# Kernel tuning notes

Measured on AMD Instinct MI355X. Metric: run time of the kernel, lower is better.

The kernel has to match this reference:

```python
import jax, jax.numpy as jnp
import numpy as np

N_NODES = 32768
N_EDGES = 524288
IN_F = 256
OUT_F = 128
NB = 4


def setup_inputs() -> dict:
    key = jax.random.key(0)
    ks = jax.random.split(key, 12)
    s_in = 1.0 / np.sqrt(IN_F)
    s_out = 1.0 / np.sqrt(OUT_F)
    s_cat = 1.0 / np.sqrt(OUT_F * NB)
    return {
        "x": jax.random.normal(ks[0], (N_NODES, IN_F), dtype=jnp.float32),
        "edge_index": jax.random.randint(ks[1], (2, N_EDGES), 0, N_NODES, dtype=jnp.int64),
        "Wb": jax.random.uniform(ks[2], (NB, IN_F, OUT_F), jnp.float32, -s_in, s_in),
        "bb": jax.random.uniform(ks[3], (NB, OUT_F), jnp.float32, -s_in, s_in),
        "W1": jax.random.uniform(ks[4], (NB, OUT_F, OUT_F), jnp.float32, -s_out, s_out),
        "b1": jax.random.uniform(ks[5], (NB, OUT_F), jnp.float32, -s_out, s_out),
        "W2": jax.random.uniform(ks[6], (NB, OUT_F, OUT_F), jnp.float32, -s_out, s_out),
        "b2": jax.random.uniform(ks[7], (NB, OUT_F), jnp.float32, -s_out, s_out),
        "branch_gates": jnp.ones((NB,), dtype=jnp.float32),
        "temperature": jnp.asarray(1.0, dtype=jnp.float32),
        "Wo": jax.random.uniform(ks[8], (OUT_F * NB, OUT_F), jnp.float32, -s_cat, s_cat),
        "bo": jax.random.uniform(ks[9], (OUT_F,), jnp.float32, -s_cat, s_cat),
    }


def _scatter_mean_step(h, row, col, inv_deg):
    # gather per-edge source features, mean-reduce onto destination nodes
    sums = jax.ops.segment_sum(h[row], col, num_segments=N_NODES)
    return sums * inv_deg


def reference(x, edge_index, Wb, bb, W1, b1, W2, b2, branch_gates, temperature, Wo, bo):
    row, col = edge_index[0], edge_index[1]
    deg = jax.ops.segment_sum(jnp.ones((N_EDGES,), x.dtype), col, num_segments=N_NODES)
    inv_deg = (1.0 / jnp.maximum(deg, 1.0))[:, None]  # empty segments -> 0 (scatter_mean semantics)

    gates = jax.nn.softmax(branch_gates / temperature)

    branch_outputs = []
    for i in range(NB):
        h = x @ Wb[i] + bb[i]                   # [N, OUT_F]
        for _ in range(i):                       # scale = scales[i % 4] = i
            h = _scatter_mean_step(h, row, col, inv_deg)
        h = jax.nn.relu(h @ W1[i] + b1[i]) @ W2[i] + b2[i]
        branch_outputs.append(h * gates[i])

    concat = jnp.concatenate(branch_outputs, axis=1)  # [N, NB*OUT_F]
    return concat @ Wo + bo
```

## Files before the change

kernel.cpp:

```cpp
#include <hip/hip_runtime.h>
#include <math.h>

#define N_NODES 32768
#define N_EDGES 524288
#define IN_F    256
#define OUT_F   128
#define NB      4
#define STRIDE  96

#define NE_BLK   256
#define CONV_BLK 1024
#define GX_BLK   2048
#define GEMM_BLK (N_NODES / 128)
#define M_BLK    (N_NODES / 256)

typedef __attribute__((ext_vector_type(8))) short bf16x8;
typedef __attribute__((ext_vector_type(4))) float f32x4;
typedef __attribute__((ext_vector_type(4))) ushort u16x4;

__device__ __forceinline__ ushort f2b(float f) {
    uint u = __float_as_uint(f);
    return (ushort)((u + 0x7fffu + ((u >> 16) & 1u)) >> 16);
}
__device__ __forceinline__ float b2f_lo(uint v) { return __uint_as_float(v << 16); }
__device__ __forceinline__ float b2f_hi(uint v) { return __uint_as_float(v & 0xffff0000u); }

__device__ __forceinline__ float softmax_gate(const float* bg, const float* temp, int i) {
    float T = temp[0];
    float mx = fmaxf(fmaxf(bg[0], bg[1]), fmaxf(bg[2], bg[3]));
    float e0 = expf((bg[0] - mx) / T), e1 = expf((bg[1] - mx) / T);
    float e2 = expf((bg[2] - mx) / T), e3 = expf((bg[3] - mx) / T);
    float s = e0 + e1 + e2 + e3;
    float ei = (i == 0) ? e0 : (i == 1) ? e1 : (i == 2) ? e2 : e3;
    return ei / s;
}

__device__ __forceinline__ int detect_i32(const int* __restrict__ ei, int* sflag) {
    if (threadIdx.x < 64) {
        unsigned long long b = __ballot(ei[2 * threadIdx.x + 1] != 0);
        if (threadIdx.x == 0) *sflag = (b != 0ull) ? 1 : 0;
    }
    __syncthreads();
    return *sflag;
}

__global__ __launch_bounds__(256) void fill_all_kernel(
    const int* __restrict__ ei, int* __restrict__ cursor, ushort* __restrict__ srcs,
    const float* __restrict__ x, ushort* __restrict__ xb,
    const float* __restrict__ Wb, const float* __restrict__ W1,
    const float* __restrict__ W2, const float* __restrict__ Wo,
    const float* __restrict__ bb, const float* __restrict__ b2,
    const float* __restrict__ bo, const float* __restrict__ bg,
    const float* __restrict__ temp,
    ushort* __restrict__ WcT, ushort* __restrict__ WzT,
    float* __restrict__ u, float* __restrict__ cvec) {
    __shared__ float smem[16 * 128];
    __shared__ int sflag;
    int b = blockIdx.x;
    int tid = threadIdx.x;
    if (b < NE_BLK) {
        int i32 = detect_i32(ei, &sflag);
#pragma unroll
        for (int it = 0; it < 8; it++) {
            int e = b * 2048 + it * 256 + tid;
            int r, c;
            if (i32 == 0) {
                r = __builtin_nontemporal_load(ei + 2 * e);
                c = __builtin_nontemporal_load(ei + 2 * (N_EDGES + e));
            } else {
                r = __builtin_nontemporal_load(ei + e);
                c = __builtin_nontemporal_load(ei + N_EDGES + e);
            }
            int slot = atomicAdd(&cursor[c], 1);
            if (slot < STRIDE) srcs[(size_t)c * STRIDE + slot] = (ushort)r;
        }
        return;
    }
    b -= NE_BLK;
    if (b < CONV_BLK) {
#pragma unroll
        for (int it = 0; it < 8; it++) {
            int idx = b * 2048 + it * 256 + tid;
            f32x4 v = __builtin_nontemporal_load((const f32x4*)x + idx);
            u16x4 o;
            o.x = f2b(v.x); o.y = f2b(v.y); o.z = f2b(v.z); o.w = f2b(v.w);
            *((u16x4*)xb + idx) = o;
        }
        return;
    }
    b -= CONV_BLK;
    int f = tid & 127, rh = tid >> 7;
    if (b < 64) {
        int i = b >> 4, k0 = (b & 15) * 16;
#pragma unroll
        for (int rr = 0; rr < 8; rr++)
            smem[(rh * 8 + rr) * 128 + f] = Wb[((size_t)i * IN_F + k0 + rh * 8 + rr) * OUT_F + f];
        __syncthreads();
        float acc[8] = {};
        const float* W1i = W1 + (size_t)i * OUT_F * OUT_F;
        for (int j = 0; j < OUT_F; j++) {
            float w1 = W1i[j * OUT_F + f];
#pragma unroll
            for (int rr = 0; rr < 8; rr++) acc[rr] += smem[(rh * 8 + rr) * 128 + j] * w1;
        }
        ushort tmp[8];
#pragma unroll
        for (int rr = 0; rr < 8; rr++) tmp[rr] = f2b(acc[rr]);
        *(uint4*)(WcT + ((size_t)i * OUT_F + f) * IN_F + k0 + rh * 8) = *(uint4*)tmp;
    } else if (b < 96) {
        int id = b - 64;
        int i = id >> 3, j0 = (id & 7) * 16;
#pragma unroll
        for (int rr = 0; rr < 8; rr++)
            smem[(rh * 8 + rr) * 128 + f] = W2[((size_t)i * OUT_F + j0 + rh * 8 + rr) * OUT_F + f];
        __syncthreads();
        float acc[8] = {};
        for (int l = 0; l < OUT_F; l++) {
            float wo = Wo[((size_t)i * OUT_F + l) * OUT_F + f];
#pragma unroll
            for (int rr = 0; rr < 8; rr++) acc[rr] += smem[(rh * 8 + rr) * 128 + l] * wo;
        }
        float g = softmax_gate(bg, temp, i);
        ushort tmp[8];
#pragma unroll
        for (int rr = 0; rr < 8; rr++) tmp[rr] = f2b(g * acc[rr]);
        *(uint4*)(WzT + (size_t)f * (NB * OUT_F) + i * OUT_F + j0 + rh * 8) = *(uint4*)tmp;
    } else {
        int id = b - 96;
        int jc = rh;
        if (id < NB) {
            int i = id;
            float partial = 0.f;
            for (int j = jc * 64; j < jc * 64 + 64; j++)
                partial += bb[i * OUT_F + j] * W1[((size_t)i * OUT_F + j) * OUT_F + f];
            smem[jc * 128 + f] = partial;
            __syncthreads();
            if (jc == 0) u[i * OUT_F + f] = smem[f] + smem[128 + f];
        } else {
            int i = id - NB;
            float partial = 0.f;
            for (int j = jc * 64; j < jc * 64 + 64; j++)
                partial += b2[i * OUT_F + j] * Wo[((size_t)i * OUT_F + j) * OUT_F + f];
            smem[jc * 128 + f] = partial;
            __syncthreads();
            if (jc == 0) {
                float tot = (smem[f] + smem[128 + f]) * softmax_gate(bg, temp, i);
                if (i == 0) tot += bo[f];
                atomicAdd(&cvec[f], tot);
            }
        }
    }
}

#define ACC4(A, V)                                                              \
    A[0] += b2f_lo(V.x); A[1] += b2f_hi(V.x);                                   \
    A[2] += b2f_lo(V.y); A[3] += b2f_hi(V.y)

#define GATHER_SLICE(INBUF, ROWSTRIDE)                                          \
    float a0[4] = {0.f,0.f,0.f,0.f};                                            \
    float a1[4] = {0.f,0.f,0.f,0.f};                                            \
    int p = s;                                                                  \
    for (; p + 12 <= e; p += 12) {                                              \
        int base = p + 6 * half;                                                \
        uint s01 = *(const uint*)(srcs + base);                                 \
        uint s23 = *(const uint*)(srcs + base + 2);                             \
        uint s45 = *(const uint*)(srcs + base + 4);                             \
        uint2 v0 = *(const uint2*)(INBUF + (size_t)(s01 & 0xffffu) * ROWSTRIDE + colOff); \
        uint2 v1 = *(const uint2*)(INBUF + (size_t)(s01 >> 16)    * ROWSTRIDE + colOff); \
        uint2 v2 = *(const uint2*)(INBUF + (size_t)(s23 & 0xffffu) * ROWSTRIDE + colOff); \
        uint2 v3 = *(const uint2*)(INBUF + (size_t)(s23 >> 16)    * ROWSTRIDE + colOff); \
        uint2 v4 = *(const uint2*)(INBUF + (size_t)(s45 & 0xffffu) * ROWSTRIDE + colOff); \
        uint2 v5 = *(const uint2*)(INBUF + (size_t)(s45 >> 16)    * ROWSTRIDE + colOff); \
        ACC4(a0, v0); ACC4(a1, v1); ACC4(a0, v2);                               \
        ACC4(a1, v3); ACC4(a0, v4); ACC4(a1, v5);                               \
    }                                                                           \
    for (; p + 4 <= e; p += 4) {                                                \
        uint ss = *(const uint*)(srcs + p + 2 * half);                          \
        uint2 v0 = *(const uint2*)(INBUF + (size_t)(ss & 0xffffu) * ROWSTRIDE + colOff); \
        uint2 v1 = *(const uint2*)(INBUF + (size_t)(ss >> 16)    * ROWSTRIDE + colOff); \
        ACC4(a0, v0); ACC4(a1, v1);                                             \
    }                                                                           \
    for (; p + half < e; p += 2) {                                              \
        int src = srcs[p + half];                                               \
        uint2 v0 = *(const uint2*)(INBUF + (size_t)src * ROWSTRIDE + colOff);   \
        ACC4(a0, v0);                                                           \
    }                                                                           \
    _Pragma("unroll") for (int k = 0; k < 4; k++) a0[k] += a1[k];               \
    _Pragma("unroll") for (int k = 0; k < 4; k++) a0[k] += __shfl_down(a0[k], 32);

#define PACK2(A, W)                                                             \
    { o.x = (uint)f2b(A[0] * W) | ((uint)f2b(A[1] * W) << 16);                  \
      o.y = (uint)f2b(A[2] * W) | ((uint)f2b(A[3] * W) << 16); }

__global__ __launch_bounds__(256, 8) void prop_x_kernel(
    const ushort* __restrict__ xb, ushort* __restrict__ X1b,
    const int* __restrict__ deg, float* __restrict__ m2,
    const ushort* __restrict__ srcs) {
    int blk = blockIdx.x;
    int tid = threadIdx.x;
    if (blk < M_BLK) {
        int n = blk * 256 + tid;
        int d = deg[n];
        int s = n * STRIDE, e = s + ((d < STRIDE) ? d : STRIDE);
        float sum = 0.f;
        for (int p = s; p < e; ++p) sum += (deg[srcs[p]] > 0) ? 1.0f : 0.0f;
        m2[n] = sum / (float)((d > 1) ? d : 1);
        return;
    }
    blk -= M_BLK;
    int pass = blk >> 11, blk2 = blk & 2047;
    int lane = tid & 63;
    int half = lane >> 5, fl = lane & 31;
    int colOff = pass * 128 + fl * 4;
    for (int i = 0; i < 4; i++) {
        int node = blk2 * 16 + i * 4 + (tid >> 6);
        int d = deg[node];
        int s = node * STRIDE, e = s + ((d < STRIDE) ? d : STRIDE);
        GATHER_SLICE(xb, IN_F);
        if (half == 0) {
            float w = 1.0f / (float)((d > 1) ? d : 1);
            uint2 o;
            PACK2(a0, w);
            *(uint2*)(X1b + (size_t)node * IN_F + colOff) = o;
        }
    }
}

__global__ __launch_bounds__(256) void gemmP_kernel(
    const ushort* __restrict__ xb, const ushort* __restrict__ X1b,
    const ushort* __restrict__ WcT, const float* __restrict__ u,
    const float* __restrict__ b1, const int* __restrict__ deg,
    ushort* __restrict__ R, ushort* __restrict__ PQ) {
    int y = blockIdx.y;
    const ushort* A = (y == 0) ? xb : X1b;
    const ushort* WT = WcT + (size_t)y * OUT_F * IN_F;
    int m0 = blockIdx.x * 128;
    __shared__ ushort As[128][72];
    __shared__ ushort Bs[128][72];
    int tid = threadIdx.x;
    int wv = tid >> 6, lane = tid & 63, quad = lane >> 4, lm = lane & 15;
    f32x4 acc[2][8];
    f32x4 zero = {0.f, 0.f, 0.f, 0.f};
#pragma unroll
    for (int i = 0; i < 2; i++)
#pragma unroll
        for (int j = 0; j < 8; j++) acc[i][j] = zero;
    for (int k0 = 0; k0 < IN_F; k0 += 64) {
        __syncthreads();
#pragma unroll
        for (int it = 0; it < 4; it++) {
            int c = tid + 256 * it;
            int r = c >> 3, c8 = c & 7;
            *(uint4*)&As[r][c8 * 8] = *(const uint4*)(A + (size_t)(m0 + r) * IN_F + k0 + c8 * 8);
            *(uint4*)&Bs[r][c8 * 8] = *(const uint4*)(WT + (size_t)r * IN_F + k0 + c8 * 8);
        }
        __syncthreads();
#pragma unroll
        for (int ks = 0; ks < 2; ks++) {
            bf16x8 af0 = *(const bf16x8*)&As[wv * 32 + lm][ks * 32 + quad * 8];
            bf16x8 af1 = *(const bf16x8*)&As[wv * 32 + 16 + lm][ks * 32 + quad * 8];
#pragma unroll
            for (int nt = 0; nt < 8; nt++) {
                bf16x8 bf = *(const bf16x8*)&Bs[nt * 16 + lm][ks * 32 + quad * 8];
                acc[0][nt] = __builtin_amdgcn_mfma_f32_16x16x32_bf16(af0, bf, acc[0][nt], 0, 0, 0);
                acc[1][nt] = __builtin_amdgcn_mfma_f32_16x16x32_bf16(af1, bf, acc[1][nt], 0, 0, 0);
            }
        }
    }
    if (y >= 2) {
        int pqoff = (y - 2) * OUT_F;
#pragma unroll
        for (int mt = 0; mt < 2; mt++)
#pragma unroll
            for (int r = 0; r < 4; r++) {
                int row = m0 + wv * 32 + mt * 16 + quad * 4 + r;
#pragma unroll
                for (int nt = 0; nt < 8; nt++) {
                    int col = nt * 16 + lm;
                    PQ[(size_t)row * IN_F + pqoff + col] = f2b(acc[mt][nt][r]);
                }
            }
    } else {
        float uv[8], bv[8];
#pragma unroll
        for (int nt = 0; nt < 8; nt++) {
            int col = nt * 16 + lm;
            uv[nt] = u[y * OUT_F + col];
            bv[nt] = b1[y * OUT_F + col];
        }
#pragma unroll
        for (int mt = 0; mt < 2; mt++)
#pragma unroll
            for (int r = 0; r < 4; r++) {
                int row = m0 + wv * 32 + mt * 16 + quad * 4 + r;
                float mval = (y == 0) ? 1.0f : ((deg[row] > 0) ? 1.0f : 0.0f);
#pragma unroll
                for (int nt = 0; nt < 8; nt++) {
                    int col = nt * 16 + lm;
                    float h = acc[mt][nt][r] + mval * uv[nt] + bv[nt];
                    R[(size_t)row * (NB * OUT_F) + y * OUT_F + col] = f2b(fmaxf(h, 0.f));
                }
            }
    }
}

__global__ __launch_bounds__(256, 8) void prop_pq_kernel(
    const ushort* __restrict__ PQ, ushort* __restrict__ R, ushort* __restrict__ Qp,
    const int* __restrict__ deg, const float* __restrict__ m2, float* __restrict__ m3,
    const float* __restrict__ u2, const float* __restrict__ b12,
    const ushort* __restrict__ srcs) {
    int blk = blockIdx.x;
    int tid = threadIdx.x;
    if (blk < M_BLK) {
        int n = blk * 256 + tid;
        int d = deg[n];
        int s = n * STRIDE, e = s + ((d < STRIDE) ? d : STRIDE);
        float sum = 0.f;
        for (int p = s; p < e; ++p) sum += m2[srcs[p]];
        m3[n] = sum / (float)((d > 1) ? d : 1);
        return;
    }
    blk -= M_BLK;
    int pass = blk >> 11, blk2 = blk & 2047;
    int lane = tid & 63;
    int half = lane >> 5, fl = lane & 31;
    int colOff = pass * 128 + fl * 4;
    for (int i = 0; i < 4; i++) {
        int node = blk2 * 16 + i * 4 + (tid >> 6);
        int d = deg[node];
        int s = node * STRIDE, e = s + ((d < STRIDE) ? d : STRIDE);
        GATHER_SLICE(PQ, IN_F);
        if (half == 0) {
            float w = 1.0f / (float)((d > 1) ? d : 1);
            if (pass == 0) {
                int col = fl * 4;
                float mv = m2[node];
                float4 ua = *(const float4*)(u2 + col);
                float4 ba = *(const float4*)(b12 + col);
                float o_[4];
                o_[0] = fmaxf(a0[0] * w + mv * ua.x + ba.x, 0.f);
                o_[1] = fmaxf(a0[1] * w + mv * ua.y + ba.y, 0.f);
                o_[2] = fmaxf(a0[2] * w + mv * ua.z + ba.z, 0.f);
                o_[3] = fmaxf(a0[3] * w + mv * ua.w + ba.w, 0.f);
                uint2 o;
                o.x = (uint)f2b(o_[0]) | ((uint)f2b(o_[1]) << 16);
                o.y = (uint)f2b(o_[2]) | ((uint)f2b(o_[3]) << 16);
                *(uint2*)(R + (size_t)node * (NB * OUT_F) + 2 * OUT_F + col) = o;
            } else {
                int col = fl * 4;
                uint2 o;
                PACK2(a0, w);
                *(uint2*)(Qp + (size_t)node * OUT_F + col) = o;
            }
        }
    }
}

__global__ __launch_bounds__(256, 8) void prop_q_kernel(
    const ushort* __restrict__ Qp, ushort* __restrict__ R,
    const int* __restrict__ deg, const float* __restrict__ m3,
    const float* __restrict__ u3, const float* __restrict__ b13,
    const ushort* __restrict__ srcs) {
    int tid = threadIdx.x;
    int lane = tid & 63;
    int half = lane >> 5, fl = lane & 31;
    int colOff = fl * 4;
    for (int i = 0; i < 4; i++) {
        int node = blockIdx.x * 16 + i * 4 + (tid >> 6);
        int d = deg[node];
        int s = node * STRIDE, e = s + ((d < STRIDE) ? d : STRIDE);
        GATHER_SLICE(Qp, OUT_F);
        if (half == 0) {
            float w = 1.0f / (float)((d > 1) ? d : 1);
            float mv = m3[node];
            int col = fl * 4;
            float4 ua = *(const float4*)(u3 + col);
            float4 ba = *(const float4*)(b13 + col);
            float o_[4];
            o_[0] = fmaxf(a0[0] * w + mv * ua.x + ba.x, 0.f);
            o_[1] = fmaxf(a0[1] * w + mv * ua.y + ba.y, 0.f);
            o_[2] = fmaxf(a0[2] * w + mv * ua.z + ba.z, 0.f);
            o_[3] = fmaxf(a0[3] * w + mv * ua.w + ba.w, 0.f);
            uint2 o;
            o.x = (uint)f2b(o_[0]) | ((uint)f2b(o_[1]) << 16);
            o.y = (uint)f2b(o_[2]) | ((uint)f2b(o_[3]) << 16);
            *(uint2*)(R + (size_t)node * (NB * OUT_F) + 3 * OUT_F + col) = o;
        }
    }
}

__global__ __launch_bounds__(256) void gemm2_mfma_kernel(
    const ushort* __restrict__ R, const ushort* __restrict__ WzT,
    const float* __restrict__ cvec, float* __restrict__ out) {
    int m0 = blockIdx.x * 128;
    const int K = NB * OUT_F;
    __shared__ ushort As[128][72];
    __shared__ ushort Bs[128][72];
    int tid = threadIdx.x;
    int wv = tid >> 6, lane = tid & 63, quad = lane >> 4, lm = lane & 15;
    f32x4 acc[2][8];
    f32x4 zero = {0.f, 0.f, 0.f, 0.f};
#pragma unroll
    for (int i = 0; i < 2; i++)
#pragma unroll
        for (int j = 0; j < 8; j++) acc[i][j] = zero;
    for (int k0 = 0; k0 < K; k0 += 64) {
        __syncthreads();
#pragma unroll
        for (int it = 0; it < 4; it++) {
            int c = tid + 256 * it;
            int r = c >> 3, c8 = c & 7;
            *(uint4*)&As[r][c8 * 8] = *(const uint4*)(R + (size_t)(m0 + r) * K + k0 + c8 * 8);
            *(uint4*)&Bs[r][c8 * 8] = *(const uint4*)(WzT + (size_t)r * K + k0 + c8 * 8);
        }
        __syncthreads();
#pragma unroll
        for (int ks = 0; ks < 2; ks++) {
            bf16x8 af0 = *(const bf16x8*)&As[wv * 32 + lm][ks * 32 + quad * 8];
            bf16x8 af1 = *(const bf16x8*)&As[wv * 32 + 16 + lm][ks * 32 + quad * 8];
#pragma unroll
            for (int nt = 0; nt < 8; nt++) {
                bf16x8 bf = *(const bf16x8*)&Bs[nt * 16 + lm][ks * 32 + quad * 8];
                acc[0][nt] = __builtin_amdgcn_mfma_f32_16x16x32_bf16(af0, bf, acc[0][nt], 0, 0, 0);
                acc[1][nt] = __builtin_amdgcn_mfma_f32_16x16x32_bf16(af1, bf, acc[1][nt], 0, 0, 0);
            }
        }
    }
    float cb[8];
#pragma unroll
    for (int nt = 0; nt < 8; nt++) cb[nt] = cvec[nt * 16 + lm];
#pragma unroll
    for (int mt = 0; mt < 2; mt++)
#pragma unroll
        for (int r = 0; r < 4; r++) {
            int row = m0 + wv * 32 + mt * 16 + quad * 4 + r;
#pragma unroll
            for (int nt = 0; nt < 8; nt++) {
                int col = nt * 16 + lm;
                __builtin_nontemporal_store(acc[mt][nt][r] + cb[nt],
                                            out + (size_t)row * OUT_F + col);
            }
        }
}

extern "C" void kernel_launch(void* const* d_in, const int* in_sizes, int n_in,
                              void* d_out, int out_size, void* d_ws, size_t ws_size,
                              hipStream_t stream) {
    const float* x    = (const float*)d_in[0];
    const int*   ei   = (const int*)d_in[1];
    const float* Wb   = (const float*)d_in[2];
    const float* bb   = (const float*)d_in[3];
    const float* W1   = (const float*)d_in[4];
    const float* b1   = (const float*)d_in[5];
    const float* W2   = (const float*)d_in[6];
    const float* b2   = (const float*)d_in[7];
    const float* bg   = (const float*)d_in[8];
    const float* temp = (const float*)d_in[9];
    const float* Wo   = (const float*)d_in[10];
    const float* bo   = (const float*)d_in[11];
    float* out = (float*)d_out;

    char* w = (char*)d_ws;
    size_t used = 0;
    auto alloc = [&](size_t bytes) {
        char* p = w + used;
        used += (bytes + 255) & ~(size_t)255;
        return p;
    };
    int*    cursor = (int*)alloc(N_NODES * 4);
    float*  cvec   = (float*)alloc(OUT_F * 4);
    ushort* srcs   = (ushort*)alloc((size_t)N_NODES * STRIDE * 2);
    float*  m2v    = (float*)alloc(N_NODES * 4);
    float*  m3v    = (float*)alloc(N_NODES * 4);
    float*  u      = (float*)alloc(NB * OUT_F * 4);
    ushort* WcT    = (ushort*)alloc((size_t)NB * IN_F * OUT_F * 2);
    ushort* WzT    = (ushort*)alloc((size_t)NB * OUT_F * OUT_F * 2);
    ushort* xb     = (ushort*)alloc((size_t)N_NODES * IN_F * 2);
    ushort* X1b    = (ushort*)alloc((size_t)N_NODES * IN_F * 2);
    ushort* PQ     = (ushort*)alloc((size_t)N_NODES * IN_F * 2);
    ushort* Qp     = (ushort*)alloc((size_t)N_NODES * OUT_F * 2);
    ushort* R      = (ushort*)alloc((size_t)N_NODES * NB * OUT_F * 2);
    if (used > ws_size) return;

    int* deg = cursor;

    hipMemsetAsync(cursor, 0, N_NODES * 4 + 512, stream);

    fill_all_kernel<<<NE_BLK + CONV_BLK + 104, 256, 0, stream>>>(
        ei, cursor, srcs, x, xb, Wb, W1, W2, Wo, bb, b2, bo, bg, temp, WcT, WzT, u, cvec);

    prop_x_kernel<<<M_BLK + 2 * GX_BLK, 256, 0, stream>>>(xb, X1b, deg, m2v, srcs);

    {
        dim3 grid(GEMM_BLK, 4);
        gemmP_kernel<<<grid, 256, 0, stream>>>(xb, X1b, WcT, u, b1, deg, R, PQ);
    }

    prop_pq_kernel<<<M_BLK + 2 * GX_BLK, 256, 0, stream>>>(
        PQ, R, Qp, deg, m2v, m3v, u + 2 * OUT_F, b1 + 2 * OUT_F, srcs);

    prop_q_kernel<<<GX_BLK, 256, 0, stream>>>(
        Qp, R, deg, m3v, u + 3 * OUT_F, b1 + 3 * OUT_F, srcs);

    gemm2_mfma_kernel<<<GEMM_BLK, 256, 0, stream>>>(R, WzT, cvec, out);
}
```

Baseline: 261.5 us.

## Split gather into 64-column slices with four edge groups per wavefront

The neighbour-gather kernels now give each wavefront a 64-column slice instead of a 128-column one, so each node's edges are spread over four 16-lane groups rather than two halves. The grids double to cover the extra column passes. Source-index loads now use nontemporal vector loads, and the partial sums are combined with an extra shuffle reduction. The aim is more memory-level parallelism per edge list and more blocks in flight. The cost is reading the edge index lists twice as often and extra shuffle work per node.

```diff
diff --git a/kernel.cpp b/kernel.cpp
--- a/kernel.cpp
+++ b/kernel.cpp
@@ -17,6 +17,7 @@
 typedef __attribute__((ext_vector_type(8))) short bf16x8;
 typedef __attribute__((ext_vector_type(4))) float f32x4;
 typedef __attribute__((ext_vector_type(4))) ushort u16x4;
+typedef __attribute__((ext_vector_type(2))) uint u32x2;
 
 __device__ __forceinline__ ushort f2b(float f) {
     uint u = __float_as_uint(f);
@@ -156,41 +157,38 @@
     A[0] += b2f_lo(V.x); A[1] += b2f_hi(V.x);                                   \
     A[2] += b2f_lo(V.y); A[3] += b2f_hi(V.y)
 
-#define GATHER_SLICE(INBUF, ROWSTRIDE)                                          \
+#define GATHER64(INBUF, ROWSTRIDE)                                              \
     float a0[4] = {0.f,0.f,0.f,0.f};                                            \
     float a1[4] = {0.f,0.f,0.f,0.f};                                            \
     int p = s;                                                                  \
-    for (; p + 12 <= e; p += 12) {                                              \
-        int base = p + 6 * half;                                                \
-        uint s01 = *(const uint*)(srcs + base);                                 \
-        uint s23 = *(const uint*)(srcs + base + 2);                             \
-        uint s45 = *(const uint*)(srcs + base + 4);                             \
-        uint2 v0 = *(const uint2*)(INBUF + (size_t)(s01 & 0xffffu) * ROWSTRIDE + colOff); \
-        uint2 v1 = *(const uint2*)(INBUF + (size_t)(s01 >> 16)    * ROWSTRIDE + colOff); \
-        uint2 v2 = *(const uint2*)(INBUF + (size_t)(s23 & 0xffffu) * ROWSTRIDE + colOff); \
-        uint2 v3 = *(const uint2*)(INBUF + (size_t)(s23 >> 16)    * ROWSTRIDE + colOff); \
-        uint2 v4 = *(const uint2*)(INBUF + (size_t)(s45 & 0xffffu) * ROWSTRIDE + colOff); \
-        uint2 v5 = *(const uint2*)(INBUF + (size_t)(s45 >> 16)    * ROWSTRIDE + colOff); \
-        ACC4(a0, v0); ACC4(a1, v1); ACC4(a0, v2);                               \
-        ACC4(a1, v3); ACC4(a0, v4); ACC4(a1, v5);                               \
+    for (; p + 16 <= e; p += 16) {                                              \
+        u32x2 sv = __builtin_nontemporal_load((const u32x2*)(srcs + p + 4 * g));\
+        uint sa = sv.x, sb = sv.y;                                              \
+        uint2 v0 = *(const uint2*)(INBUF + (size_t)(sa & 0xffffu) * ROWSTRIDE + colOff); \
+        uint2 v1 = *(const uint2*)(INBUF + (size_t)(sa >> 16)     * ROWSTRIDE + colOff); \
+        uint2 v2 = *(const uint2*)(INBUF + (size_t)(sb & 0xffffu) * ROWSTRIDE + colOff); \
+        uint2 v3 = *(const uint2*)(INBUF + (size_t)(sb >> 16)     * ROWSTRIDE + colOff); \
+        ACC4(a0, v0); ACC4(a1, v1); ACC4(a0, v2); ACC4(a1, v3);                 \
+    }                                                                           \
+    for (; p + 8 <= e; p += 8) {                                                \
+        uint sa = __builtin_nontemporal_load((const uint*)(srcs + p + 2 * g));  \
+        uint2 v0 = *(const uint2*)(INBUF + (size_t)(sa & 0xffffu) * ROWSTRIDE + colOff); \
+        uint2 v1 = *(const uint2*)(INBUF + (size_t)(sa >> 16)     * ROWSTRIDE + colOff); \
+        ACC4(a0, v0); ACC4(a1, v1);                                             \
     }                                                                           \
     for (; p + 4 <= e; p += 4) {                                                \
-        uint ss = *(const uint*)(srcs + p + 2 * half);                          \
-        uint2 v0 = *(const uint2*)(INBUF + (size_t)(ss & 0xffffu) * ROWSTRIDE + colOff); \
-        uint2 v1 = *(const uint2*)(INBUF + (size_t)(ss >> 16)    * ROWSTRIDE + colOff); \
-        ACC4(a0, v0); ACC4(a1, v1);                                             \
-    }                                                                           \
-    for (; p + half < e; p += 2) {                                              \
-        int src = srcs[p + half];                                               \
+        int src = srcs[p + g];                                                  \
         uint2 v0 = *(const uint2*)(INBUF + (size_t)src * ROWSTRIDE + colOff);   \
         ACC4(a0, v0);                                                           \
     }                                                                           \
+    if (p + g < e) {                                                            \
+        int src = srcs[p + g];                                                  \
+        uint2 v0 = *(const uint2*)(INBUF + (size_t)src * ROWSTRIDE + colOff);   \
+        ACC4(a1, v0);                                                           \
+    }                                                                           \
     _Pragma("unroll") for (int k = 0; k < 4; k++) a0[k] += a1[k];               \
-    _Pragma("unroll") for (int k = 0; k < 4; k++) a0[k] += __shfl_down(a0[k], 32);
-
-#define PACK2(A, W)                                                             \
-    { o.x = (uint)f2b(A[0] * W) | ((uint)f2b(A[1] * W) << 16);                  \
-      o.y = (uint)f2b(A[2] * W) | ((uint)f2b(A[3] * W) << 16); }
+    _Pragma("unroll") for (int k = 0; k < 4; k++) a0[k] += __shfl_down(a0[k], 32); \
+    _Pragma("unroll") for (int k = 0; k < 4; k++) a0[k] += __shfl_down(a0[k], 16);
 
 __global__ __launch_bounds__(256, 8) void prop_x_kernel(
     const ushort* __restrict__ xb, ushort* __restrict__ X1b,
@@ -210,17 +208,18 @@
     blk -= M_BLK;
     int pass = blk >> 11, blk2 = blk & 2047;
     int lane = tid & 63;
-    int half = lane >> 5, fl = lane & 31;
-    int colOff = pass * 128 + fl * 4;
+    int g = lane >> 4, fl = lane & 15;
+    int colOff = pass * 64 + fl * 4;
     for (int i = 0; i < 4; i++) {
         int node = blk2 * 16 + i * 4 + (tid >> 6);
         int d = deg[node];
         int s = node * STRIDE, e = s + ((d < STRIDE) ? d : STRIDE);
-        GATHER_SLICE(xb, IN_F);
-        if (half == 0) {
+        GATHER64(xb, IN_F);
+        if (lane < 16) {
             float w = 1.0f / (float)((d > 1) ? d : 1);
             uint2 o;
-            PACK2(a0, w);
+            o.x = (uint)f2b(a0[0] * w) | ((uint)f2b(a0[1] * w) << 16);
+            o.y = (uint)f2b(a0[2] * w) | ((uint)f2b(a0[3] * w) << 16);
             *(uint2*)(X1b + (size_t)node * IN_F + colOff) = o;
         }
     }
@@ -323,17 +322,17 @@
     blk -= M_BLK;
     int pass = blk >> 11, blk2 = blk & 2047;
     int lane = tid & 63;
-    int half = lane >> 5, fl = lane & 31;
-    int colOff = pass * 128 + fl * 4;
+    int g = lane >> 4, fl = lane & 15;
+    int colOff = pass * 64 + fl * 4;
     for (int i = 0; i < 4; i++) {
         int node = blk2 * 16 + i * 4 + (tid >> 6);
         int d = deg[node];
         int s = node * STRIDE, e = s + ((d < STRIDE) ? d : STRIDE);
-        GATHER_SLICE(PQ, IN_F);
-        if (half == 0) {
+        GATHER64(PQ, IN_F);
+        if (lane < 16) {
             float w = 1.0f / (float)((d > 1) ? d : 1);
-            if (pass == 0) {
-                int col = fl * 4;
+            if (pass < 2) {
+                int col = colOff;
                 float mv = m2[node];
                 float4 ua = *(const float4*)(u2 + col);
                 float4 ba = *(const float4*)(b12 + col);
@@ -347,9 +346,10 @@
                 o.y = (uint)f2b(o_[2]) | ((uint)f2b(o_[3]) << 16);
                 *(uint2*)(R + (size_t)node * (NB * OUT_F) + 2 * OUT_F + col) = o;
             } else {
-                int col = fl * 4;
+                int col = colOff - 128;
                 uint2 o;
-                PACK2(a0, w);
+                o.x = (uint)f2b(a0[0] * w) | ((uint)f2b(a0[1] * w) << 16);
+                o.y = (uint)f2b(a0[2] * w) | ((uint)f2b(a0[3] * w) << 16);
                 *(uint2*)(Qp + (size_t)node * OUT_F + col) = o;
             }
         }
@@ -361,19 +361,21 @@
     const int* __restrict__ deg, const float* __restrict__ m3,
     const float* __restrict__ u3, const float* __restrict__ b13,
     const ushort* __restrict__ srcs) {
+    int blk = blockIdx.x;
     int tid = threadIdx.x;
+    int pass = blk >> 11, blk2 = blk & 2047;
     int lane = tid & 63;
-    int half = lane >> 5, fl = lane & 31;
-    int colOff = fl * 4;
+    int g = lane >> 4, fl = lane & 15;
+    int colOff = pass * 64 + fl * 4;
     for (int i = 0; i < 4; i++) {
-        int node = blockIdx.x * 16 + i * 4 + (tid >> 6);
+        int node = blk2 * 16 + i * 4 + (tid >> 6);
         int d = deg[node];
         int s = node * STRIDE, e = s + ((d < STRIDE) ? d : STRIDE);
-        GATHER_SLICE(Qp, OUT_F);
-        if (half == 0) {
+        GATHER64(Qp, OUT_F);
+        if (lane < 16) {
             float w = 1.0f / (float)((d > 1) ? d : 1);
             float mv = m3[node];
-            int col = fl * 4;
+            int col = colOff;
             float4 ua = *(const float4*)(u3 + col);
             float4 ba = *(const float4*)(b13 + col);
             float o_[4];
@@ -489,17 +491,17 @@
     fill_all_kernel<<<NE_BLK + CONV_BLK + 104, 256, 0, stream>>>(
         ei, cursor, srcs, x, xb, Wb, W1, W2, Wo, bb, b2, bo, bg, temp, WcT, WzT, u, cvec);
 
-    prop_x_kernel<<<M_BLK + 2 * GX_BLK, 256, 0, stream>>>(xb, X1b, deg, m2v, srcs);
+    prop_x_kernel<<<M_BLK + 4 * GX_BLK, 256, 0, stream>>>(xb, X1b, deg, m2v, srcs);
 
     {
         dim3 grid(GEMM_BLK, 4);
         gemmP_kernel<<<grid, 256, 0, stream>>>(xb, X1b, WcT, u, b1, deg, R, PQ);
     }
 
-    prop_pq_kernel<<<M_BLK + 2 * GX_BLK, 256, 0, stream>>>(
+    prop_pq_kernel<<<M_BLK + 4 * GX_BLK, 256, 0, stream>>>(
         PQ, R, Qp, deg, m2v, m3v, u + 2 * OUT_F, b1 + 2 * OUT_F, srcs);
 
-    prop_q_kernel<<<GX_BLK, 256, 0, stream>>>(
+    prop_q_kernel<<<2 * GX_BLK, 256, 0, stream>>>(
         Qp, R, deg, m3v, u + 3 * OUT_F, b1 + 3 * OUT_F, srcs);
 
     gemm2_mfma_kernel<<<GEMM_BLK, 256, 0, stream>>>(R, WzT, cvec, out);
```

Measured after the change: 306.2 us. +17.1%, slower.

## Move branch-0 GEMM into prop_x kernel to overlap with gather

Applied to the files above, without the earlier changes.

The branch-0 dense GEMM (x @ Wc0 plus bias and ReLU) no longer runs in gemmP. It now runs as extra blocks at the front of prop_x_kernel, each block doing a register-only MFMA tile that reads A and B straight from global memory without LDS staging. The intent is for the compute-bound GEMM to overlap with the memory-bound gather blocks and to shrink the gemmP grid from 4 to 3 branches. The cost is a less efficient GEMM with no LDS reuse of the weights, plus extra register pressure in a kernel launched with launch_bounds(256,8).

```diff
diff --git a/kernel.cpp b/kernel.cpp
--- a/kernel.cpp
+++ b/kernel.cpp
@@ -12,6 +12,7 @@
 #define CONV_BLK 1024
 #define GX_BLK   2048
 #define GEMM_BLK (N_NODES / 128)
+#define GEMM0_BLK (N_NODES / 64)
 #define M_BLK    (N_NODES / 256)
 
 typedef __attribute__((ext_vector_type(8))) short bf16x8;
@@ -195,9 +196,41 @@
 __global__ __launch_bounds__(256, 8) void prop_x_kernel(
     const ushort* __restrict__ xb, ushort* __restrict__ X1b,
     const int* __restrict__ deg, float* __restrict__ m2,
-    const ushort* __restrict__ srcs) {
+    const ushort* __restrict__ srcs,
+    const ushort* __restrict__ WcT, const float* __restrict__ u,
+    const float* __restrict__ b1, ushort* __restrict__ R) {
     int blk = blockIdx.x;
     int tid = threadIdx.x;
+    if (blk < GEMM0_BLK) {
+        int wv = tid >> 6, lane = tid & 63, quad = lane >> 4, lm = lane & 15;
+        int row16 = blk * 64 + wv * 16;
+        f32x4 acc[8];
+        f32x4 zero = {0.f, 0.f, 0.f, 0.f};
+#pragma unroll
+        for (int nt = 0; nt < 8; nt++) acc[nt] = zero;
+        const ushort* Arow = xb + (size_t)(row16 + lm) * IN_F;
+#pragma unroll
+        for (int k0 = 0; k0 < IN_F; k0 += 32) {
+            bf16x8 af = *(const bf16x8*)(Arow + k0 + quad * 8);
+#pragma unroll
+            for (int nt = 0; nt < 8; nt++) {
+                bf16x8 bf = *(const bf16x8*)(WcT + (size_t)(nt * 16 + lm) * IN_F + k0 + quad * 8);
+                acc[nt] = __builtin_amdgcn_mfma_f32_16x16x32_bf16(af, bf, acc[nt], 0, 0, 0);
+            }
+        }
+#pragma unroll
+        for (int r = 0; r < 4; r++) {
+            int row = row16 + quad * 4 + r;
+#pragma unroll
+            for (int nt = 0; nt < 8; nt++) {
+                int col = nt * 16 + lm;
+                float h = acc[nt][r] + u[col] + b1[col];
+                R[(size_t)row * (NB * OUT_F) + col] = f2b(fmaxf(h, 0.f));
+            }
+        }
+        return;
+    }
+    blk -= GEMM0_BLK;
     if (blk < M_BLK) {
         int n = blk * 256 + tid;
         int d = deg[n];
@@ -231,8 +264,8 @@
     const ushort* __restrict__ WcT, const float* __restrict__ u,
     const float* __restrict__ b1, const int* __restrict__ deg,
     ushort* __restrict__ R, ushort* __restrict__ PQ) {
-    int y = blockIdx.y;
-    const ushort* A = (y == 0) ? xb : X1b;
+    int y = blockIdx.y + 1;
+    const ushort* A = X1b;
     const ushort* WT = WcT + (size_t)y * OUT_F * IN_F;
     int m0 = blockIdx.x * 128;
     __shared__ ushort As[128][72];
@@ -293,7 +326,7 @@
 #pragma unroll
             for (int r = 0; r < 4; r++) {
                 int row = m0 + wv * 32 + mt * 16 + quad * 4 + r;
-                float mval = (y == 0) ? 1.0f : ((deg[row] > 0) ? 1.0f : 0.0f);
+                float mval = (deg[row] > 0) ? 1.0f : 0.0f;
 #pragma unroll
                 for (int nt = 0; nt < 8; nt++) {
                     int col = nt * 16 + lm;
@@ -489,10 +522,11 @@
     fill_all_kernel<<<NE_BLK + CONV_BLK + 104, 256, 0, stream>>>(
         ei, cursor, srcs, x, xb, Wb, W1, W2, Wo, bb, b2, bo, bg, temp, WcT, WzT, u, cvec);
 
-    prop_x_kernel<<<M_BLK + 2 * GX_BLK, 256, 0, stream>>>(xb, X1b, deg, m2v, srcs);
+    prop_x_kernel<<<GEMM0_BLK + M_BLK + 2 * GX_BLK, 256, 0, stream>>>(
+        xb, X1b, deg, m2v, srcs, WcT, u, b1, R);
 
     {
-        dim3 grid(GEMM_BLK, 4);
+        dim3 grid(GEMM_BLK, 3);
         gemmP_kernel<<<grid, 256, 0, stream>>>(xb, X1b, WcT, u, b1, deg, R, PQ);
     }
 
```

Result: slower. 279.9 us (+7.1%).
